# Kernel optimization log

Measured on AMD Instinct MI355X. Metric: run time of the kernel, lower is better.

## Reference

```python
import jax, jax.numpy as jnp
import numpy as np

D_MODEL, NHEAD, D_FF, N_EXP, TOP_K = 1024, 16, 4096, 8, 2
EPS = 1e-5


def setup_inputs() -> dict:
    key = jax.random.key(0)
    ks = jax.random.split(key, 16)
    s = 0.02
    B, S, d = 4, 1024, D_MODEL
    return {
        'src': jax.random.normal(ks[0], (B, S, d), jnp.float32),
        'in_proj_w': jax.random.normal(ks[1], (3 * d, d), jnp.float32) * s,
        'in_proj_b': jnp.zeros((3 * d,), jnp.float32),
        'out_proj_w': jax.random.normal(ks[2], (d, d), jnp.float32) * s,
        'out_proj_b': jnp.zeros((d,), jnp.float32),
        'ln1_g': jnp.ones((d,), jnp.float32),
        'ln1_b': jnp.zeros((d,), jnp.float32),
        'router_w': jax.random.normal(ks[3], (N_EXP, d), jnp.float32) * s,
        'router_b': jnp.zeros((N_EXP,), jnp.float32),
        'w1': jax.random.normal(ks[4], (N_EXP, d, D_FF), jnp.float32) * s,
        'b1': jnp.zeros((N_EXP, D_FF), jnp.float32),
        'w2': jax.random.normal(ks[5], (N_EXP, D_FF, d), jnp.float32) * s,
        'b2': jnp.zeros((N_EXP, d), jnp.float32),
        'ln2_g': jnp.ones((d,), jnp.float32),
        'ln2_b': jnp.zeros((d,), jnp.float32),
    }


def layer_norm(x, g, b):
    mu = x.mean(-1, keepdims=True)
    var = ((x - mu) ** 2).mean(-1, keepdims=True)
    return (x - mu) * jax.lax.rsqrt(var + EPS) * g + b


def mha(x, wqkv, bqkv, wo, bo):
    B, S, d = x.shape
    dh = d // NHEAD
    qkv = x @ wqkv.T + bqkv                      # [B,S,3d]
    q, k, v = jnp.split(qkv, 3, axis=-1)
    def heads(t):
        return t.reshape(B, S, NHEAD, dh).transpose(0, 2, 1, 3)  # [B,h,S,dh]
    q, k, v = heads(q), heads(k), heads(v)
    scores = jnp.einsum('bhqd,bhkd->bhqk', q, k) / jnp.sqrt(jnp.float32(dh))
    a = jax.nn.softmax(scores, axis=-1)
    o = jnp.einsum('bhqk,bhkd->bhqd', a, v)
    o = o.transpose(0, 2, 1, 3).reshape(B, S, d)
    return o @ wo.T + bo


def moe(x, router_w, router_b, w1, b1, w2, b2):
    B, S, d = x.shape
    xt = x.reshape(-1, d)                         # [T,d]
    logits = xt @ router_w.T + router_b           # [T,E]
    probs = jax.nn.softmax(logits, axis=-1)
    topv, topi = jax.lax.top_k(probs, TOP_K)      # [T,k]
    mask = jax.nn.one_hot(topi, N_EXP, dtype=xt.dtype).sum(1)  # [T,E] 0/1
    gates = probs * mask
    gates = gates / gates.sum(-1, keepdims=True)  # renormalized top-k weights
    # dense expert compute, weighted combine (zero gate => no contribution)
    h = jax.nn.relu(jnp.einsum('td,edf->etf', xt, w1) + b1[:, None, :])
    y = jnp.einsum('etf,efd->etd', h, w2) + b2[:, None, :]
    out = jnp.einsum('te,etd->td', gates, y).reshape(B, S, d)
    # Switch-style load balancing loss
    f = mask.mean(0) / TOP_K                      # fraction of assignments
    P = probs.mean(0)                             # mean router prob
    lb = jnp.float32(N_EXP) * jnp.sum(f * P)
    return out, lb


def reference(src, in_proj_w, in_proj_b, out_proj_w, out_proj_b, ln1_g, ln1_b,
              router_w, router_b, w1, b1, w2, b2, ln2_g, ln2_b):
    a = mha(src, in_proj_w, in_proj_b, out_proj_w, out_proj_b)
    x = layer_norm(src + a, ln1_g, ln1_b)
    m, lb = moe(x, router_w, router_b, w1, b1, w2, b2)
    x = layer_norm(x + m, ln2_g, ln2_b)
    return x, lb
```

## Files before the change

kernel.cpp:

```cpp
#include <hip/hip_runtime.h>


typedef __attribute__((ext_vector_type(8))) short short8;
typedef __attribute__((ext_vector_type(4))) short short4v;
typedef __attribute__((ext_vector_type(4))) float floatx4;

#define TOKENS 4096
#define DMODEL 1024
#define NHEADS 16
#define DHEAD  64
#define DFF    4096
#define NEXP   8
#define SEQ    1024
#define NPAIR  64

__device__ inline short f2bf(float f) {
  unsigned u = __builtin_bit_cast(unsigned, f);
  unsigned r = (u + 0x7fffu + ((u >> 16) & 1u)) >> 16;
  return (short)r;
}
__device__ inline float bf2f(short h) {
  return __builtin_bit_cast(float, ((unsigned)(unsigned short)h) << 16);
}

__device__ inline void gload16(const short* g, short* l) {
  __builtin_amdgcn_global_load_lds(
      (const __attribute__((address_space(1))) unsigned int*)g,
      (__attribute__((address_space(3))) unsigned int*)l, 16, 0, 0);
}

template<int BM, int BN, int WTM, int WTN, int EPI, int AMODE, bool RELU, bool SPLIT>
__global__ void __launch_bounds__((BM / WTM) * (BN / WTN) * 64)
gemm_nt(const short* __restrict__ Ab, const short* __restrict__ Abl, int lda, long sA,
        const short* __restrict__ Bb, const short* __restrict__ Bbl, int ldb, long sB,
        void* __restrict__ Cb, int ldc, long sC,
        int M, int N, int K, float scale,
        const float* __restrict__ bias, int sBias,
        const float* __restrict__ srcadd,
        const int* __restrict__ tokList,
        const int* __restrict__ counts,
        const int* __restrict__ offsets)
{
  constexpr int WROWS = BM / WTM;
  constexpr int WCOLS = BN / WTN;
  constexpr int NW = WROWS * WCOLS;
  constexpr int MT = WTM / 16;
  constexpr int NT = WTN / 16;
  constexpr int ISSA = (BM / 16) / NW;
  constexpr int ISSB = (BN / 16) / NW;
  constexpr int PL = SPLIT ? 2 : 1;
  constexpr int ABUF = PL * BM * 32;
  constexpr int BBUF = PL * BN * 32;

  int xw, yw, zw;
  if (AMODE != 0) {
    int flat = blockIdx.x + gridDim.x * (blockIdx.y + gridDim.y * blockIdx.z);
    zw = flat & 7;
    int m = flat >> 3;
    xw = m % gridDim.x;
    yw = m / gridDim.x;
  } else {
    int nwg = gridDim.x * gridDim.y;
    int f2 = blockIdx.x + gridDim.x * blockIdx.y;
    int cpx = nwg >> 3;
    int g = (f2 & 7) * cpx + (f2 >> 3);
    xw = g % gridDim.x;
    yw = g / gridDim.x;
    zw = blockIdx.z;
  }

  const int z = zw;
  int Mt = M;
  int rowbase = 0;
  const int* tl = nullptr;
  if (AMODE != 0) {
    Mt = counts[z];
    if (xw * BM >= Mt) return;
    if (AMODE == 1) tl = tokList + offsets[z];
    else rowbase = offsets[z];
  }

  const short* A = Ab + (long)z * sA;
  const short* Al = SPLIT ? (Abl + (long)z * sA) : nullptr;
  const short* B = Bb + (long)z * sB;
  const short* Bl = SPLIT ? (Bbl + (long)z * sB) : nullptr;
  const int tid = threadIdx.x;
  const int lane = tid & 63;
  const int w = tid >> 6;
  const int wrow = w % WROWS;
  const int wcol = w / WROWS;
  const int m0 = xw * BM;
  const int n0 = yw * BN;

  __shared__ __align__(16) short As[2 * ABUF];
  __shared__ __align__(16) short Bs[2 * BBUF];

  const int l4 = lane >> 2;
  const int lc = (lane & 3) ^ (l4 & 3) ^ ((lane >> 4) & 3);
  long agp[ISSA]; int albase[ISSA];
#pragma unroll
  for (int r = 0; r < ISSA; ++r) {
    int seg = w * ISSA + r;
    int row = seg * 16 + l4;
    int grow;
    if (AMODE == 0) grow = m0 + row;
    else if (AMODE == 1) grow = tl[min(m0 + row, Mt - 1)];
    else grow = rowbase + min(m0 + row, Mt - 1);
    agp[r] = (long)grow * lda + lc * 8;
    albase[r] = seg * 512;
  }
  long bgp[ISSB]; int blbase[ISSB];
#pragma unroll
  for (int r = 0; r < ISSB; ++r) {
    int seg = w * ISSB + r;
    int row = seg * 16 + l4;
    bgp[r] = (long)(n0 + row) * ldb + lc * 8;
    blbase[r] = seg * 512;
  }

  floatx4 acc[MT][NT];
#pragma unroll
  for (int i = 0; i < MT; ++i)
#pragma unroll
    for (int j = 0; j < NT; ++j) acc[i][j] = floatx4{0.f, 0.f, 0.f, 0.f};

  const int am = wrow * WTM + (lane & 15);
  const int bn = wcol * WTN + (lane & 15);
  const int ac = lane >> 4;
  const int aro = am * 32 + ((ac ^ (am & 3) ^ ((am >> 2) & 3)) << 3);
  const int bro = bn * 32 + ((ac ^ (bn & 3) ^ ((bn >> 2) & 3)) << 3);

  auto stage = [&](int buf, int k0) {
    short* Ad = &As[buf * ABUF];
    short* Bd = &Bs[buf * BBUF];
#pragma unroll
    for (int r = 0; r < ISSA; ++r) gload16(A + agp[r] + k0, Ad + albase[r]);
#pragma unroll
    for (int r = 0; r < ISSB; ++r) gload16(B + bgp[r] + k0, Bd + blbase[r]);
    if (SPLIT) {
#pragma unroll
      for (int r = 0; r < ISSA; ++r) gload16(Al + agp[r] + k0, Ad + BM * 32 + albase[r]);
#pragma unroll
      for (int r = 0; r < ISSB; ++r) gload16(Bl + bgp[r] + k0, Bd + BN * 32 + blbase[r]);
    }
  };

  auto compute = [&](int buf) {
    const short* Ar = &As[buf * ABUF];
    const short* Br = &Bs[buf * BBUF];
    short8 afh[MT], bfh[NT];
#pragma unroll
    for (int i = 0; i < MT; ++i) afh[i] = *(const short8*)&Ar[aro + i * 512];
#pragma unroll
    for (int j = 0; j < NT; ++j) bfh[j] = *(const short8*)&Br[bro + j * 512];
    if (SPLIT) {
      short8 afl[MT], bfl[NT];
#pragma unroll
      for (int i = 0; i < MT; ++i) afl[i] = *(const short8*)&Ar[BM * 32 + aro + i * 512];
#pragma unroll
      for (int j = 0; j < NT; ++j) bfl[j] = *(const short8*)&Br[BN * 32 + bro + j * 512];
#pragma unroll
      for (int i = 0; i < MT; ++i)
#pragma unroll
        for (int j = 0; j < NT; ++j) {
          acc[i][j] = __builtin_amdgcn_mfma_f32_16x16x32_bf16(afh[i], bfh[j], acc[i][j], 0, 0, 0);
          acc[i][j] = __builtin_amdgcn_mfma_f32_16x16x32_bf16(afh[i], bfl[j], acc[i][j], 0, 0, 0);
          acc[i][j] = __builtin_amdgcn_mfma_f32_16x16x32_bf16(afl[i], bfh[j], acc[i][j], 0, 0, 0);
        }
    } else {
#pragma unroll
      for (int i = 0; i < MT; ++i)
#pragma unroll
        for (int j = 0; j < NT; ++j)
          acc[i][j] = __builtin_amdgcn_mfma_f32_16x16x32_bf16(afh[i], bfh[j], acc[i][j], 0, 0, 0);
    }
  };

  const int ntile = K >> 5;
  stage(0, 0);
  __syncthreads();
  int cur = 0;
  for (int t = 0; t < ntile - 1; ++t) {
    compute(cur);
    stage(cur ^ 1, (t + 1) << 5);
    __syncthreads();
    cur ^= 1;
  }
  compute(cur);

  const float* bz = bias ? (bias + (long)z * sBias) : nullptr;
#pragma unroll
  for (int i = 0; i < MT; ++i) {
    int rt = wrow * WTM + i * 16 + ((lane >> 4) << 2);
#pragma unroll
    for (int j = 0; j < NT; ++j) {
      int col = n0 + wcol * WTN + j * 16 + (lane & 15);
      float badd = bz ? bz[col] : 0.f;
      floatx4 v = acc[i][j];
#pragma unroll
      for (int q = 0; q < 4; ++q) {
        int r = m0 + rt + q;
        if (AMODE != 0 && r >= Mt) break;
        long orow = (AMODE == 1) ? ((long)offsets[z] + r)
                  : (AMODE == 2) ? ((long)rowbase + r) : (long)r;
        float val = v[q] * scale + badd;
        if (RELU) val = fmaxf(val, 0.f);
        if (EPI == 0) {
          ((short*)Cb)[(long)z * sC + orow * ldc + col] = f2bf(val);
        } else {
          float* Cf = (float*)Cb + (long)z * sC;
          if (srcadd) val += srcadd[orow * ldc + col];
          Cf[orow * ldc + col] = val;
        }
      }
    }
  }
}

__global__ void __launch_bounds__(256)
fused_attn(const short* __restrict__ Qh, const short* __restrict__ Ql,
           const short* __restrict__ Kh, const short* __restrict__ Kl,
           const short* __restrict__ Vh, const short* __restrict__ Vl,
           short* __restrict__ Ohi, short* __restrict__ Olo)
{
  const int f = blockIdx.x + 8 * blockIdx.z;
  const int pair = (f & 7) + ((f >> 6) << 3);
  const int qt = (f >> 3) & 7;
  const long pb = (long)pair * 65536;
  const int lane = threadIdx.x & 63;
  const int w = threadIdx.x >> 6;
  const int qb0 = qt * 128;

  __shared__ __align__(16) short Ksh[4096], Ksl[4096];
  __shared__ __align__(16) short Vsh[4096], Vsl[4096];
  __shared__ __align__(16) short Ph[4][32 * 72], Pl[4][32 * 72];

  short8 qfh[2][2], qfl[2][2];
#pragma unroll
  for (int i = 0; i < 2; ++i)
#pragma unroll
    for (int kt = 0; kt < 2; ++kt) {
      long qoff = pb + (long)(qb0 + w * 32 + i * 16 + (lane & 15)) * 64
                + (lane >> 4) * 8 + kt * 32;
      qfh[i][kt] = *(const short8*)&Qh[qoff];
      qfl[i][kt] = *(const short8*)&Ql[qoff];
    }

  floatx4 oacc[2][4];
#pragma unroll
  for (int i = 0; i < 2; ++i)
#pragma unroll
    for (int jd = 0; jd < 4; ++jd) oacc[i][jd] = floatx4{0.f, 0.f, 0.f, 0.f};
  float mrow[2][4], lrow[2][4];
#pragma unroll
  for (int i = 0; i < 2; ++i)
#pragma unroll
    for (int q = 0; q < 4; ++q) { mrow[i][q] = -1e30f; lrow[i][q] = 0.f; }

  const int r8 = lane >> 3, pc8 = lane & 7;
  const int lc8 = ((pc8 ^ r8) & 7) * 8;

  for (int t = 0; t < 16; ++t) {
    const int kv0 = t * 64;
    __syncthreads();
#pragma unroll
    for (int s = 0; s < 2; ++s) {
      int seg = w * 2 + s;
      long krow = kv0 + seg * 8 + r8;
      gload16(&Kh[pb + krow * 64 + lc8], &Ksh[seg * 512]);
      gload16(&Kl[pb + krow * 64 + lc8], &Ksl[seg * 512]);
      long drow = seg * 8 + r8;
      gload16(&Vh[pb + drow * 1024 + kv0 + lc8], &Vsh[seg * 512]);
      gload16(&Vl[pb + drow * 1024 + kv0 + lc8], &Vsl[seg * 512]);
    }
    __syncthreads();

    floatx4 sacc[2][4];
#pragma unroll
    for (int i = 0; i < 2; ++i)
#pragma unroll
      for (int j = 0; j < 4; ++j) sacc[i][j] = floatx4{0.f, 0.f, 0.f, 0.f};
#pragma unroll
    for (int j = 0; j < 4; ++j) {
      int rr = j * 16 + (lane & 15);
      int base = rr * 64, rsw = rr & 7;
#pragma unroll
      for (int kt = 0; kt < 2; ++kt) {
        int kc = (lane >> 4) + kt * 4;
        int off = base + ((kc ^ rsw) << 3);
        short8 kh8 = *(const short8*)&Ksh[off];
        short8 kl8 = *(const short8*)&Ksl[off];
#pragma unroll
        for (int i = 0; i < 2; ++i) {
          sacc[i][j] = __builtin_amdgcn_mfma_f32_16x16x32_bf16(qfh[i][kt], kh8, sacc[i][j], 0, 0, 0);
          sacc[i][j] = __builtin_amdgcn_mfma_f32_16x16x32_bf16(qfh[i][kt], kl8, sacc[i][j], 0, 0, 0);
          sacc[i][j] = __builtin_amdgcn_mfma_f32_16x16x32_bf16(qfl[i][kt], kh8, sacc[i][j], 0, 0, 0);
        }
      }
    }
#pragma unroll
    for (int i = 0; i < 2; ++i)
#pragma unroll
      for (int j = 0; j < 4; ++j) sacc[i][j] *= 0.125f;

#pragma unroll
    for (int i = 0; i < 2; ++i)
#pragma unroll
      for (int q = 0; q < 4; ++q) {
        float tm = fmaxf(fmaxf(sacc[i][0][q], sacc[i][1][q]),
                         fmaxf(sacc[i][2][q], sacc[i][3][q]));
#pragma unroll
        for (int msk = 1; msk < 16; msk <<= 1) tm = fmaxf(tm, __shfl_xor(tm, msk));
        float mold = mrow[i][q];
        float mn = fmaxf(mold, tm);
        float c = expf(mold - mn);
        mrow[i][q] = mn;
        float ts = 0.f;
#pragma unroll
        for (int j = 0; j < 4; ++j) {
          float p = expf(sacc[i][j][q] - mn);
          sacc[i][j][q] = p;
          ts += p;
        }
#pragma unroll
        for (int msk = 1; msk < 16; msk <<= 1) ts += __shfl_xor(ts, msk);
        lrow[i][q] = lrow[i][q] * c + ts;
#pragma unroll
        for (int jd = 0; jd < 4; ++jd) oacc[i][jd][q] *= c;
      }

    short* php = Ph[w];
    short* plp = Pl[w];
#pragma unroll
    for (int i = 0; i < 2; ++i)
#pragma unroll
      for (int j = 0; j < 4; ++j)
#pragma unroll
        for (int q = 0; q < 4; ++q) {
          float p = sacc[i][j][q];
          short ph_ = f2bf(p);
          short pl_ = f2bf(p - bf2f(ph_));
          int row = i * 16 + ((lane >> 4) << 2) + q;
          int col = j * 16 + (lane & 15);
          php[row * 72 + col] = ph_;
          plp[row * 72 + col] = pl_;
        }
    asm volatile("s_waitcnt lgkmcnt(0)" ::: "memory");
    __builtin_amdgcn_sched_barrier(0);

    short8 pah[2][2], pal[2][2];
#pragma unroll
    for (int i = 0; i < 2; ++i)
#pragma unroll
      for (int kt = 0; kt < 2; ++kt) {
        int off = (i * 16 + (lane & 15)) * 72 + (lane >> 4) * 8 + kt * 32;
        pah[i][kt] = *(const short8*)&php[off];
        pal[i][kt] = *(const short8*)&plp[off];
      }
#pragma unroll
    for (int jd = 0; jd < 4; ++jd) {
      int rr = jd * 16 + (lane & 15);
      int base = rr * 64, rsw = rr & 7;
#pragma unroll
      for (int kt = 0; kt < 2; ++kt) {
        int kc = (lane >> 4) + kt * 4;
        int off = base + ((kc ^ rsw) << 3);
        short8 vh8 = *(const short8*)&Vsh[off];
        short8 vl8 = *(const short8*)&Vsl[off];
#pragma unroll
        for (int i = 0; i < 2; ++i) {
          oacc[i][jd] = __builtin_amdgcn_mfma_f32_16x16x32_bf16(pah[i][kt], vh8, oacc[i][jd], 0, 0, 0);
          oacc[i][jd] = __builtin_amdgcn_mfma_f32_16x16x32_bf16(pah[i][kt], vl8, oacc[i][jd], 0, 0, 0);
          oacc[i][jd] = __builtin_amdgcn_mfma_f32_16x16x32_bf16(pal[i][kt], vh8, oacc[i][jd], 0, 0, 0);
        }
      }
    }
  }

  const int b = pair >> 4, hh = pair & 15;
#pragma unroll
  for (int i = 0; i < 2; ++i)
#pragma unroll
    for (int q = 0; q < 4; ++q) {
      float inv = 1.f / lrow[i][q];
      int qrow = qb0 + w * 32 + i * 16 + ((lane >> 4) << 2) + q;
      long obase = (long)(b * 1024 + qrow) * 1024 + hh * 64;
#pragma unroll
      for (int jd = 0; jd < 4; ++jd) {
        float v = oacc[i][jd][q] * inv;
        short vh_ = f2bf(v);
        long oi = obase + jd * 16 + (lane & 15);
        Ohi[oi] = vh_;
        Olo[oi] = f2bf(v - bf2f(vh_));
      }
    }
}

__global__ void split_bf16(const float* __restrict__ src, short* __restrict__ hi,
                           short* __restrict__ lo, int n) {
  int i = (blockIdx.x * 256 + threadIdx.x) * 4;
  if (i >= n) return;
  float4 v = *(const float4*)(src + i);
  short h0 = f2bf(v.x), h1 = f2bf(v.y), h2 = f2bf(v.z), h3 = f2bf(v.w);
  short4v oh = { h0, h1, h2, h3 };
  short4v ol = { f2bf(v.x - bf2f(h0)), f2bf(v.y - bf2f(h1)),
                 f2bf(v.z - bf2f(h2)), f2bf(v.w - bf2f(h3)) };
  *(short4v*)(hi + i) = oh;
  *(short4v*)(lo + i) = ol;
}

__global__ void transpose_bf16(const float* __restrict__ src, short* __restrict__ dst,
                               int R, int C) {
  __shared__ float t[64][65];
  long zoff = (long)blockIdx.z * R * C;
  const float* s = src + zoff;
  short* d = dst + zoff;
  int r0 = blockIdx.y * 64, c0 = blockIdx.x * 64;
  int tid = threadIdx.x;
#pragma unroll
  for (int i = 0; i < 16; ++i) {
    int flat = i * 256 + tid;
    int r = flat >> 6, c = flat & 63;
    t[r][c] = s[(long)(r0 + r) * C + c0 + c];
  }
  __syncthreads();
#pragma unroll
  for (int i = 0; i < 16; ++i) {
    int flat = i * 256 + tid;
    int c = flat >> 6, r = flat & 63;
    d[(long)(c0 + c) * R + r0 + r] = f2bf(t[r][c]);
  }
}

__global__ void repack_qkv_split(const float* __restrict__ qkv,
                                 short* __restrict__ Qh, short* __restrict__ Ql,
                                 short* __restrict__ Kh, short* __restrict__ Kl,
                                 short* __restrict__ Vh, short* __restrict__ Vl) {
  long idx = (long)blockIdx.x * 256 + threadIdx.x;
  int t = (int)(idx / 3072), c = (int)(idx % 3072);
  int sec = c >> 10, within = c & 1023;
  int h = within >> 6, di = within & 63;
  int b = t >> 10, s = t & 1023;
  int g = b * NHEADS + h;
  float v = qkv[idx];
  short vh = f2bf(v);
  short vl = f2bf(v - bf2f(vh));
  if (sec == 2) {
    long vo = (long)g * 65536 + di * 1024 + s;
    Vh[vo] = vh; Vl[vo] = vl;
  } else {
    long qo = (long)g * 65536 + s * 64 + di;
    if (sec == 0) { Qh[qo] = vh; Ql[qo] = vl; }
    else          { Kh[qo] = vh; Kl[qo] = vl; }
  }
}

__global__ void ln_rows(const float* __restrict__ x, const float* __restrict__ g,
                        const float* __restrict__ b, float* __restrict__ of,
                        short* __restrict__ ob) {
  __shared__ float ws1[4], ws2[4];
  long row = blockIdx.x;
  const float* p = x + row * 1024;
  int tid = threadIdx.x;
  float4 v = *(const float4*)(p + tid * 4);
  float s = v.x + v.y + v.z + v.w;
  float s2 = v.x * v.x + v.y * v.y + v.z * v.z + v.w * v.w;
  for (int m = 1; m < 64; m <<= 1) { s += __shfl_xor(s, m); s2 += __shfl_xor(s2, m); }
  if ((tid & 63) == 0) { ws1[tid >> 6] = s; ws2[tid >> 6] = s2; }
  __syncthreads();
  s = ws1[0] + ws1[1] + ws1[2] + ws1[3];
  s2 = ws2[0] + ws2[1] + ws2[2] + ws2[3];
  float mean = s * (1.f / 1024.f);
  float var = s2 * (1.f / 1024.f) - mean * mean;
  float rstd = rsqrtf(var + 1e-5f);
  float4 gg = *(const float4*)(g + tid * 4);
  float4 bb = *(const float4*)(b + tid * 4);
  float y0 = (v.x - mean) * rstd * gg.x + bb.x;
  float y1 = (v.y - mean) * rstd * gg.y + bb.y;
  float y2 = (v.z - mean) * rstd * gg.z + bb.z;
  float y3 = (v.w - mean) * rstd * gg.w + bb.w;
  if (of) { float4 o = { y0, y1, y2, y3 }; *(float4*)(of + row * 1024 + tid * 4) = o; }
  if (ob) { short4v o = { f2bf(y0), f2bf(y1), f2bf(y2), f2bf(y3) }; *(short4v*)(ob + row * 1024 + tid * 4) = o; }
}

__global__ void combine_ln2(const float* __restrict__ accum, const float* __restrict__ y,
                            const int* __restrict__ pos1, const int* __restrict__ pos2,
                            const float* __restrict__ g1a, const float* __restrict__ g2a,
                            const float* __restrict__ gn, const float* __restrict__ bn,
                            float* __restrict__ out) {
  __shared__ float ws1[4], ws2[4];
  int t = blockIdx.x;
  int tid = threadIdx.x;
  const float* a = accum + (long)t * 1024;
  const float* y1 = y + (long)pos1[t] * 1024;
  const float* y2 = y + (long)pos2[t] * 1024;
  float G1 = g1a[t], G2 = g2a[t];
  float4 va = *(const float4*)(a + tid * 4);
  float4 v1 = *(const float4*)(y1 + tid * 4);
  float4 v2 = *(const float4*)(y2 + tid * 4);
  float x0 = va.x + G1 * v1.x + G2 * v2.x;
  float x1 = va.y + G1 * v1.y + G2 * v2.y;
  float x2 = va.z + G1 * v1.z + G2 * v2.z;
  float x3 = va.w + G1 * v1.w + G2 * v2.w;
  float s = x0 + x1 + x2 + x3;
  float s2 = x0 * x0 + x1 * x1 + x2 * x2 + x3 * x3;
  for (int m = 1; m < 64; m <<= 1) { s += __shfl_xor(s, m); s2 += __shfl_xor(s2, m); }
  if ((tid & 63) == 0) { ws1[tid >> 6] = s; ws2[tid >> 6] = s2; }
  __syncthreads();
  s = ws1[0] + ws1[1] + ws1[2] + ws1[3];
  s2 = ws2[0] + ws2[1] + ws2[2] + ws2[3];
  float mean = s * (1.f / 1024.f);
  float var = s2 * (1.f / 1024.f) - mean * mean;
  float rstd = rsqrtf(var + 1e-5f);
  float4 gg = *(const float4*)(gn + tid * 4);
  float4 bb = *(const float4*)(bn + tid * 4);
  float4 o = { (x0 - mean) * rstd * gg.x + bb.x,
               (x1 - mean) * rstd * gg.y + bb.y,
               (x2 - mean) * rstd * gg.z + bb.z,
               (x3 - mean) * rstd * gg.w + bb.w };
  *(float4*)(out + (long)t * 1024 + tid * 4) = o;
}

__global__ void router_compute(const float* __restrict__ x, const float* __restrict__ rw,
                               const float* __restrict__ rb,
                               int* __restrict__ top1, int* __restrict__ top2,
                               float* __restrict__ g1o, float* __restrict__ g2o,
                               float* __restrict__ partialP) {
  __shared__ float pp[4][8];
  int w = threadIdx.x >> 6, lane = threadIdx.x & 63;
  int t = blockIdx.x * 4 + w;
  const float* xp = x + (long)t * 1024;
  float xv[16];
#pragma unroll
  for (int i = 0; i < 16; ++i) xv[i] = xp[lane + i * 64];
  float logit[8];
#pragma unroll
  for (int e = 0; e < 8; ++e) {
    const float* wp = rw + e * 1024;
    double a = 0.0;
#pragma unroll
    for (int i = 0; i < 16; ++i) a += (double)xv[i] * (double)wp[lane + i * 64];
    for (int m = 1; m < 64; m <<= 1) a += __shfl_xor(a, m);
    logit[e] = (float)a + rb[e];
  }
  float mx = logit[0];
#pragma unroll
  for (int e = 1; e < 8; ++e) mx = fmaxf(mx, logit[e]);
  float pe[8], sum = 0.f;
#pragma unroll
  for (int e = 0; e < 8; ++e) { pe[e] = expf(logit[e] - mx); sum += pe[e]; }
  float inv = 1.f / sum;
#pragma unroll
  for (int e = 0; e < 8; ++e) pe[e] *= inv;
  int i1 = 0;
#pragma unroll
  for (int e = 1; e < 8; ++e) if (pe[e] > pe[i1]) i1 = e;
  int i2 = (i1 == 0) ? 1 : 0;
#pragma unroll
  for (int e = 0; e < 8; ++e) if (e != i1 && pe[e] > pe[i2]) i2 = e;
  float denom = pe[i1] + pe[i2];
  if (lane == 0) {
    top1[t] = i1; top2[t] = i2;
    g1o[t] = pe[i1] / denom; g2o[t] = pe[i2] / denom;
#pragma unroll
    for (int e = 0; e < 8; ++e) pp[w][e] = pe[e];
  }
  __syncthreads();
  if (threadIdx.x < 8) {
    partialP[(long)blockIdx.x * 8 + threadIdx.x] =
        pp[0][threadIdx.x] + pp[1][threadIdx.x] + pp[2][threadIdx.x] + pp[3][threadIdx.x];
  }
}

__global__ void __launch_bounds__(1024) router_finalize(
    const float* __restrict__ partialP,
    const int* __restrict__ top1, const int* __restrict__ top2,
    int* __restrict__ counts, int* __restrict__ eoff_out,
    int* __restrict__ tokList, int* __restrict__ pos1, int* __restrict__ pos2,
    float* __restrict__ lb_out) {
  __shared__ float redP[16][8];
  __shared__ int wtot[16][8];
  __shared__ int tot[8], eoff[8];
  __shared__ float psum[8];
  int tid = threadIdx.x;
  int lane = tid & 63, wv = tid >> 6;

  float p[8];
#pragma unroll
  for (int e = 0; e < 8; ++e) p[e] = partialP[(long)tid * 8 + e];
  for (int m = 1; m < 64; m <<= 1)
#pragma unroll
    for (int e = 0; e < 8; ++e) p[e] += __shfl_xor(p[e], m);
  if (lane == 0)
#pragma unroll
    for (int e = 0; e < 8; ++e) redP[wv][e] = p[e];

  int c[8] = {0, 0, 0, 0, 0, 0, 0, 0};
  int expid[8];
#pragma unroll
  for (int j = 0; j < 8; ++j) {
    int i = tid * 8 + j;
    int t = i >> 1;
    int e = (i & 1) ? top2[t] : top1[t];
    expid[j] = e;
    c[e]++;
  }
  int inc[8];
#pragma unroll
  for (int e = 0; e < 8; ++e) inc[e] = c[e];
  for (int d = 1; d < 64; d <<= 1) {
#pragma unroll
    for (int e = 0; e < 8; ++e) {
      int o = __shfl_up(inc[e], d);
      if (lane >= d) inc[e] += o;
    }
  }
  if (lane == 63)
#pragma unroll
    for (int e = 0; e < 8; ++e) wtot[wv][e] = inc[e];
  __syncthreads();
  if (tid < 8) {
    int run = 0;
#pragma unroll
    for (int w = 0; w < 16; ++w) { int v = wtot[w][tid]; wtot[w][tid] = run; run += v; }
    tot[tid] = run;
    float s = 0.f;
#pragma unroll
    for (int w = 0; w < 16; ++w) s += redP[w][tid];
    psum[tid] = s;
  }
  __syncthreads();
  if (tid == 0) {
    int off = 0;
#pragma unroll
    for (int e = 0; e < 8; ++e) { eoff[e] = off; off += tot[e]; }
  }
  __syncthreads();
  int base[8], c2[8] = {0, 0, 0, 0, 0, 0, 0, 0};
#pragma unroll
  for (int e = 0; e < 8; ++e) base[e] = eoff[e] + wtot[wv][e] + inc[e] - c[e];
#pragma unroll
  for (int j = 0; j < 8; ++j) {
    int i = tid * 8 + j;
    int t = i >> 1;
    int e = expid[j];
    int dest = base[e] + c2[e]++;
    tokList[dest] = t;
    if (i & 1) pos2[t] = dest; else pos1[t] = dest;
  }
  if (tid < 8) { counts[tid] = tot[tid]; eoff_out[tid] = eoff[tid]; }
  if (tid == 0) {
    float lb = 0.f;
#pragma unroll
    for (int e = 0; e < 8; ++e)
      lb += ((float)tot[e] / 8192.f) * (psum[e] / 4096.f);
    *lb_out = 8.f * lb;
  }
}

__global__ void sentinel_kernel(float* out, int n) {
  if (threadIdx.x == 0) { out[0] = 1e9f; out[n - 1] = 1e9f; }
}

extern "C" void kernel_launch(void* const* d_in, const int* in_sizes, int n_in,
                              void* d_out, int out_size, void* d_ws, size_t ws_size,
                              hipStream_t stream) {
  const float* src        = (const float*)d_in[0];
  const float* in_proj_w  = (const float*)d_in[1];
  const float* in_proj_b  = (const float*)d_in[2];
  const float* out_proj_w = (const float*)d_in[3];
  const float* out_proj_b = (const float*)d_in[4];
  const float* ln1_g      = (const float*)d_in[5];
  const float* ln1_b      = (const float*)d_in[6];
  const float* router_w   = (const float*)d_in[7];
  const float* router_b   = (const float*)d_in[8];
  const float* w1         = (const float*)d_in[9];
  const float* b1         = (const float*)d_in[10];
  const float* w2         = (const float*)d_in[11];
  const float* b2         = (const float*)d_in[12];
  const float* ln2_g      = (const float*)d_in[13];
  const float* ln2_b      = (const float*)d_in[14];
  float* out = (float*)d_out;

  char* ws = (char*)d_ws;
  size_t off = 0;
  auto alloc = [&](size_t bytes) -> char* {
    char* p = ws + off;
    off += (bytes + 255) & ~(size_t)255;
    return p;
  };
  char*  blockW = alloc(8ll * (DFF * DMODEL + DMODEL * DFF) * 2);
  short* Qh = (short*)(blockW + 0ll  * 1024 * 1024);
  short* Ql = (short*)(blockW + 8ll  * 1024 * 1024);
  short* Kh = (short*)(blockW + 16ll * 1024 * 1024);
  short* Kl = (short*)(blockW + 24ll * 1024 * 1024);
  short* Vh = (short*)(blockW + 32ll * 1024 * 1024);
  short* Vl = (short*)(blockW + 40ll * 1024 * 1024);
  short* w1t = (short*)blockW;
  short* w2t = (short*)(blockW + 8ll * DFF * DMODEL * 2);
  short* winh  = (short*)alloc(3072ll * 1024 * 2);
  short* winl  = (short*)alloc(3072ll * 1024 * 2);
  short* wouth = (short*)alloc(1024ll * 1024 * 2);
  short* woutl = (short*)alloc(1024ll * 1024 * 2);
  short* xh    = (short*)alloc((long)TOKENS * DMODEL * 2);
  short* xl    = (short*)alloc((long)TOKENS * DMODEL * 2);
  char*  reg1  = alloc((long)TOKENS * 3072 * 4);
  float* qkvf  = (float*)reg1;
  short* Ohi   = (short*)(reg1 + 16ll * 1024 * 1024);
  short* Olo   = (short*)(reg1 + 24ll * 1024 * 1024);
  float* x1    = (float*)(reg1 + 32ll * 1024 * 1024);
  float* y     = (float*)reg1;
  char*  reg2  = alloc(16ll * 1024 * 1024 * 4);
  short* h      = (short*)reg2;
  short* x1nbf = (short*)alloc((long)TOKENS * DMODEL * 2);
  float* accum = (float*)alloc((long)TOKENS * DMODEL * 4);
  float* partialP = (float*)alloc(1024 * 8 * 4);
  int*   top1   = (int*)alloc(TOKENS * 4);
  int*   top2   = (int*)alloc(TOKENS * 4);
  float* g1a    = (float*)alloc(TOKENS * 4);
  float* g2a    = (float*)alloc(TOKENS * 4);
  int*   pos1   = (int*)alloc(TOKENS * 4);
  int*   pos2   = (int*)alloc(TOKENS * 4);
  int*   counts = (int*)alloc(32);
  int*   eoff   = (int*)alloc(32);
  int*   tokList = (int*)alloc(2 * TOKENS * 4);
  size_t needed = off;

  if (ws_size < needed) {
    sentinel_kernel<<<1, 64, 0, stream>>>(out, out_size);
    return;
  }

  split_bf16<<<3072 * 1024 / 1024, 256, 0, stream>>>(in_proj_w, winh, winl, 3072 * 1024);
  split_bf16<<<1024 * 1024 / 1024, 256, 0, stream>>>(out_proj_w, wouth, woutl, 1024 * 1024);
  split_bf16<<<TOKENS * DMODEL / 1024, 256, 0, stream>>>(src, xh, xl, TOKENS * DMODEL);

  gemm_nt<128, 128, 64, 64, 1, 0, false, true><<<dim3(32, 24, 1), 256, 0, stream>>>(
      xh, xl, 1024, 0, winh, winl, 1024, 0, qkvf, 3072, 0,
      TOKENS, 3072, 1024, 1.f, in_proj_b, 0, nullptr, nullptr, nullptr, nullptr);
  repack_qkv_split<<<(int)((long)TOKENS * 3072 / 256), 256, 0, stream>>>(qkvf, Qh, Ql, Kh, Kl, Vh, Vl);

  fused_attn<<<dim3(8, 1, 64), 256, 0, stream>>>(Qh, Ql, Kh, Kl, Vh, Vl, Ohi, Olo);

  transpose_bf16<<<dim3(DFF / 64, DMODEL / 64, 8), 256, 0, stream>>>(w1, w1t, DMODEL, DFF);
  transpose_bf16<<<dim3(DMODEL / 64, DFF / 64, 8), 256, 0, stream>>>(w2, w2t, DFF, DMODEL);

  gemm_nt<128, 128, 64, 64, 1, 0, false, true><<<dim3(32, 8, 1), 256, 0, stream>>>(
      Ohi, Olo, 1024, 0, wouth, woutl, 1024, 0, x1, 1024, 0,
      TOKENS, 1024, 1024, 1.f, out_proj_b, 0, src, nullptr, nullptr, nullptr);

  ln_rows<<<TOKENS, 256, 0, stream>>>(x1, ln1_g, ln1_b, accum, x1nbf);

  router_compute<<<TOKENS / 4, 256, 0, stream>>>(accum, router_w, router_b,
                                                 top1, top2, g1a, g2a, partialP);
  router_finalize<<<1, 1024, 0, stream>>>(partialP, top1, top2, counts, eoff,
                                          tokList, pos1, pos2, out + (out_size - 1));

  gemm_nt<128, 128, 64, 64, 0, 1, true, false><<<dim3(32, 32, 8), 256, 0, stream>>>(
      x1nbf, nullptr, 1024, 0, w1t, nullptr, 1024, (long)DFF * DMODEL, h, DFF, 0,
      0, DFF, 1024, 1.f, b1, DFF, nullptr, tokList, counts, eoff);

  gemm_nt<128, 128, 64, 64, 1, 2, false, false><<<dim3(32, 8, 8), 256, 0, stream>>>(
      h, nullptr, DFF, 0, w2t, nullptr, DFF, (long)DMODEL * DFF, y, 1024, 0,
      0, DMODEL, DFF, 1.f, b2, DMODEL, nullptr, tokList, counts, eoff);

  combine_ln2<<<TOKENS, 256, 0, stream>>>(accum, y, pos1, pos2, g1a, g2a,
                                          ln2_g, ln2_b, out);
}
```

Before: 956.1 us.

## Fuse QKV head repack into GEMM epilogue and stage bf16 stores via LDS

The QKV projection GEMM now writes the split hi/lo bf16 Q, K and V head layouts directly from its epilogue (EPI==2), so the fp32 qkv buffer and the separate repack kernel go away. This saves writing and re-reading a 48MB fp32 intermediate plus one launch. The bf16 epilogue (EPI==0) is also changed to stage each tile through shared memory and emit 16-byte vectorized row stores instead of scattered 2-byte stores. The fused QKV epilogue still does scattered 2-byte stores, and the V transpose layout gives poorly coalesced writes.

```diff
diff --git a/kernel.cpp b/kernel.cpp
--- a/kernel.cpp
+++ b/kernel.cpp
@@ -188,29 +188,80 @@
   }
   compute(cur);
 
-  const float* bz = bias ? (bias + (long)z * sBias) : nullptr;
-#pragma unroll
-  for (int i = 0; i < MT; ++i) {
-    int rt = wrow * WTM + i * 16 + ((lane >> 4) << 2);
-#pragma unroll
-    for (int j = 0; j < NT; ++j) {
-      int col = n0 + wcol * WTN + j * 16 + (lane & 15);
-      float badd = bz ? bz[col] : 0.f;
-      floatx4 v = acc[i][j];
-#pragma unroll
-      for (int q = 0; q < 4; ++q) {
-        int r = m0 + rt + q;
-        if (AMODE != 0 && r >= Mt) break;
+  if constexpr (EPI == 0) {
+    short* CT = As;
+    const float* bzz = bias ? (bias + (long)z * sBias) : nullptr;
+#pragma unroll
+    for (int p = 0; p < 2; ++p) {
+      __syncthreads();
+      if (wrow == p) {
+#pragma unroll
+        for (int i = 0; i < MT; ++i) {
+          int rl = i * 16 + ((lane >> 4) << 2);
+#pragma unroll
+          for (int j = 0; j < NT; ++j) {
+            int cl = wcol * WTN + j * 16 + (lane & 15);
+            float badd = bzz ? bzz[n0 + cl] : 0.f;
+            floatx4 v = acc[i][j];
+#pragma unroll
+            for (int q = 0; q < 4; ++q) {
+              float val = v[q] * scale + badd;
+              if (RELU) val = fmaxf(val, 0.f);
+              CT[(rl + q) * BN + cl] = f2bf(val);
+            }
+          }
+        }
+      }
+      __syncthreads();
+      int fb = tid * 32;
+#pragma unroll
+      for (int u = 0; u < 4; ++u) {
+        int fs = fb + u * 8;
+        int rloc = fs >> 7;
+        int cloc = fs & 127;
+        int r = m0 + p * 64 + rloc;
+        if (AMODE != 0 && r >= Mt) continue;
         long orow = (AMODE == 1) ? ((long)offsets[z] + r)
                   : (AMODE == 2) ? ((long)rowbase + r) : (long)r;
-        float val = v[q] * scale + badd;
-        if (RELU) val = fmaxf(val, 0.f);
-        if (EPI == 0) {
-          ((short*)Cb)[(long)z * sC + orow * ldc + col] = f2bf(val);
-        } else {
-          float* Cf = (float*)Cb + (long)z * sC;
-          if (srcadd) val += srcadd[orow * ldc + col];
-          Cf[orow * ldc + col] = val;
+        *(short8*)((short*)Cb + (long)z * sC + orow * ldc + n0 + cloc) =
+            *(const short8*)&CT[fs];
+      }
+    }
+  } else {
+    const float* bz = bias ? (bias + (long)z * sBias) : nullptr;
+#pragma unroll
+    for (int i = 0; i < MT; ++i) {
+      int rt = wrow * WTM + i * 16 + ((lane >> 4) << 2);
+#pragma unroll
+      for (int j = 0; j < NT; ++j) {
+        int col = n0 + wcol * WTN + j * 16 + (lane & 15);
+        float badd = bz ? bz[col] : 0.f;
+        floatx4 v = acc[i][j];
+#pragma unroll
+        for (int q = 0; q < 4; ++q) {
+          int r = m0 + rt + q;
+          if (AMODE != 0 && r >= Mt) break;
+          float val = v[q] * scale + badd;
+          if (RELU) val = fmaxf(val, 0.f);
+          if constexpr (EPI == 2) {
+            short* base = (short*)Cb;
+            int sec = col >> 10, within = col & 1023;
+            int hh = within >> 6, di = within & 63;
+            int g = (r >> 10) * 16 + hh;
+            int s = r & 1023;
+            long off = (sec == 2) ? ((long)g * 65536 + di * 1024 + s)
+                                  : ((long)g * 65536 + s * 64 + di);
+            long plane = (long)sec * 8388608;
+            short vh = f2bf(val);
+            base[plane + off] = vh;
+            base[plane + 4194304 + off] = f2bf(val - bf2f(vh));
+          } else {
+            long orow = (AMODE == 1) ? ((long)offsets[z] + r)
+                      : (AMODE == 2) ? ((long)rowbase + r) : (long)r;
+            float* Cf = (float*)Cb + (long)z * sC;
+            if (srcadd) val += srcadd[orow * ldc + col];
+            Cf[orow * ldc + col] = val;
+          }
         }
       }
     }
@@ -429,29 +480,6 @@
     int flat = i * 256 + tid;
     int c = flat >> 6, r = flat & 63;
     d[(long)(c0 + c) * R + r0 + r] = f2bf(t[r][c]);
-  }
-}
-
-__global__ void repack_qkv_split(const float* __restrict__ qkv,
-                                 short* __restrict__ Qh, short* __restrict__ Ql,
-                                 short* __restrict__ Kh, short* __restrict__ Kl,
-                                 short* __restrict__ Vh, short* __restrict__ Vl) {
-  long idx = (long)blockIdx.x * 256 + threadIdx.x;
-  int t = (int)(idx / 3072), c = (int)(idx % 3072);
-  int sec = c >> 10, within = c & 1023;
-  int h = within >> 6, di = within & 63;
-  int b = t >> 10, s = t & 1023;
-  int g = b * NHEADS + h;
-  float v = qkv[idx];
-  short vh = f2bf(v);
-  short vl = f2bf(v - bf2f(vh));
-  if (sec == 2) {
-    long vo = (long)g * 65536 + di * 1024 + s;
-    Vh[vo] = vh; Vl[vo] = vl;
-  } else {
-    long qo = (long)g * 65536 + s * 64 + di;
-    if (sec == 0) { Qh[qo] = vh; Ql[qo] = vl; }
-    else          { Kh[qo] = vh; Kl[qo] = vl; }
   }
 }
 
@@ -705,7 +733,6 @@
   short* xh    = (short*)alloc((long)TOKENS * DMODEL * 2);
   short* xl    = (short*)alloc((long)TOKENS * DMODEL * 2);
   char*  reg1  = alloc((long)TOKENS * 3072 * 4);
-  float* qkvf  = (float*)reg1;
   short* Ohi   = (short*)(reg1 + 16ll * 1024 * 1024);
   short* Olo   = (short*)(reg1 + 24ll * 1024 * 1024);
   float* x1    = (float*)(reg1 + 32ll * 1024 * 1024);
@@ -735,10 +762,9 @@
   split_bf16<<<1024 * 1024 / 1024, 256, 0, stream>>>(out_proj_w, wouth, woutl, 1024 * 1024);
   split_bf16<<<TOKENS * DMODEL / 1024, 256, 0, stream>>>(src, xh, xl, TOKENS * DMODEL);
 
-  gemm_nt<128, 128, 64, 64, 1, 0, false, true><<<dim3(32, 24, 1), 256, 0, stream>>>(
-      xh, xl, 1024, 0, winh, winl, 1024, 0, qkvf, 3072, 0,
+  gemm_nt<128, 128, 64, 64, 2, 0, false, true><<<dim3(32, 24, 1), 256, 0, stream>>>(
+      xh, xl, 1024, 0, winh, winl, 1024, 0, (void*)Qh, 0, 0,
       TOKENS, 3072, 1024, 1.f, in_proj_b, 0, nullptr, nullptr, nullptr, nullptr);
-  repack_qkv_split<<<(int)((long)TOKENS * 3072 / 256), 256, 0, stream>>>(qkvf, Qh, Ql, Kh, Kl, Vh, Vl);
 
   fused_attn<<<dim3(8, 1, 64), 256, 0, stream>>>(Qh, Ql, Kh, Kl, Vh, Vl, Ohi, Olo);
 
```

New measurement: 963.8 us. No clear change (+0.8%).
